# Kernel tuning notes

Hardware: AMD Instinct MI355X
Metric: run time of the kernel (lower is better)

The kernel has to match this reference:

```python
import jax, jax.numpy as jnp
import numpy as np
from jax import lax

B, C, H, W = 32, 3, 128, 128
HP, WP = 7, 7          # feature map after 4 stride-2 valid 3x3 convs on 128
GH, GW = 32, 32        # glimpse shape
BN_EPS = 1e-5


def _conv(x, w, b, stride):
    y = lax.conv_general_dilated(x, w, (stride, stride), 'VALID',
                                 dimension_numbers=('NCHW', 'OIHW', 'NCHW'))
    return y + b[None, :, None, None]


def _bn(x, g, be):
    # training-mode BatchNorm2d: biased batch stats over (N,H,W)
    m = x.mean(axis=(0, 2, 3), keepdims=True)
    v = ((x - m) ** 2).mean(axis=(0, 2, 3), keepdims=True)
    return g[None, :, None, None] * (x - m) * lax.rsqrt(v + BN_EPS) + be[None, :, None, None]


def setup_inputs() -> dict:
    key = jax.random.key(0)
    ks = jax.random.split(key, 16)
    def w_init(k, shape):
        fan_in = shape[1] * shape[2] * shape[3]
        return (jax.random.normal(k, shape, jnp.float32) / np.sqrt(fan_in)).astype(jnp.float32)
    chans = [3, 64, 64, 64, 64]
    inp = {}
    inp['img'] = jax.random.normal(ks[0], (B, C, H, W), jnp.float32)
    inp['eps_scale'] = jax.random.normal(ks[1], (B, HP, WP, 2), jnp.float32)
    inp['eps_shift'] = jax.random.normal(ks[2], (B, HP, WP, 2), jnp.float32)
    for i in range(4):
        inp[f'w{i+1}'] = w_init(ks[3 + i], (chans[i + 1], chans[i], 3, 3))
        inp[f'b{i+1}'] = jnp.zeros((chans[i + 1],), jnp.float32)
        inp[f'g{i+1}'] = jnp.ones((chans[i + 1],), jnp.float32)
        inp[f'be{i+1}'] = jnp.zeros((chans[i + 1],), jnp.float32)
    inp['wp'] = w_init(ks[10], (64, 64, 1, 1)); inp['bp'] = jnp.zeros((64,), jnp.float32)
    inp['wz'] = w_init(ks[11], (11, 64, 1, 1)); inp['bz'] = jnp.zeros((11,), jnp.float32)
    return inp


def reference(img, eps_scale, eps_shift,
              w1, b1, g1, be1, w2, b2, g2, be2,
              w3, b3, g3, be3, w4, b4, g4, be4,
              wp, bp, wz, bz):
    h = img
    for (w, b, g, be) in ((w1, b1, g1, be1), (w2, b2, g2, be2),
                          (w3, b3, g3, be3), (w4, b4, g4, be4)):
        h = jax.nn.elu(_bn(_conv(h, w, b, 2), g, be))
    feats = jax.nn.elu(_conv(h, wp, bp, 1))            # [B,64,HP,WP]

    # --- znet and latent splits (only scale/shift affect returned glimpses) ---
    Z = _conv(feats, wz, bz, 1).transpose(0, 2, 3, 1)  # [B,HP,WP,11]
    smean, slogstd = Z[..., 3:5], Z[..., 5:7]
    shmean, shlogstd = Z[..., 7:9], Z[..., 9:11]
    z_scale = smean + jax.nn.softplus(slogstd) * eps_scale
    z_shift = shmean + jax.nn.softplus(shlogstd) * eps_shift

    glimpse_hw = jnp.array([GH, GW], jnp.float32)
    image_hw = jnp.array([H, W], jnp.float32)
    fmap_hw = jnp.array([HP, WP], jnp.float32)
    scale_img = jax.nn.sigmoid(z_scale) * glimpse_hw / image_hw   # [B,HP,WP,2] (h,w)
    shift_img = jax.nn.sigmoid(z_shift) / fmap_hw                 # [B,HP,WP,2] (i,j)

    ii = jnp.arange(HP, dtype=jnp.float32) / HP
    jj = jnp.arange(WP, dtype=jnp.float32) / WP
    ij = jnp.stack(jnp.meshgrid(ii, jj, indexing='ij'), axis=-1)  # [HP,WP,2]
    center = (ij[None] + shift_img) * 2.0 - 1.0                   # [B,HP,WP,2] in [-1,1]

    K = HP * WP
    th = scale_img[..., 0].reshape(B, K)   # height scale
    tw = scale_img[..., 1].reshape(B, K)   # width scale
    tx = center[..., 0].reshape(B, K)      # row (y) center
    ty = center[..., 1].reshape(B, K)      # col (x) center

    # affine_grid (align_corners=False) base coords; theta = [[tw,0,ty],[0,th,tx]]
    xb = (2.0 * jnp.arange(GW, dtype=jnp.float32) + 1.0) / GW - 1.0
    yb = (2.0 * jnp.arange(GH, dtype=jnp.float32) + 1.0) / GH - 1.0
    ixn = tw[:, :, None, None] * xb[None, None, None, :] + ty[:, :, None, None]  # [B,K,1,GW]
    iyn = th[:, :, None, None] * yb[None, None, :, None] + tx[:, :, None, None]  # [B,K,GH,1]
    # normalized -> pixel coords (align_corners=False)
    px = jnp.broadcast_to(((ixn + 1.0) * W - 1.0) * 0.5, (B, K, GH, GW))
    py = jnp.broadcast_to(((iyn + 1.0) * H - 1.0) * 0.5, (B, K, GH, GW))

    def sample_one(im, pxb, pyb):
        # im [C,H,W]; pxb/pyb [K,GH,GW]; bilinear, zero padding
        x0 = jnp.floor(pxb); y0 = jnp.floor(pyb)
        wx1 = pxb - x0; wy1 = pyb - y0
        x0i = x0.astype(jnp.int32); y0i = y0.astype(jnp.int32)
        x1i = x0i + 1; y1i = y0i + 1
        def g(yi, xi):
            m = ((xi >= 0) & (xi < W) & (yi >= 0) & (yi < H)).astype(im.dtype)
            v = im[:, jnp.clip(yi, 0, H - 1), jnp.clip(xi, 0, W - 1)]  # [C,K,GH,GW]
            return v * m[None]
        return (g(y0i, x0i) * ((1 - wy1) * (1 - wx1))[None]
                + g(y0i, x1i) * ((1 - wy1) * wx1)[None]
                + g(y1i, x0i) * (wy1 * (1 - wx1))[None]
                + g(y1i, x1i) * (wy1 * wx1)[None])

    xs = jax.vmap(sample_one)(img, px, py)            # [B,C,K,GH,GW]
    return xs.transpose(0, 2, 1, 3, 4).reshape(B * K, C, GH, GW)
```

## Files before the change

kernel.cpp:

```cpp
#include <hip/hip_runtime.h>
#include <math.h>

#define BATCH 32

__device__ __forceinline__ float eluf(float v) { return v > 0.f ? v : expm1f(v); }
__device__ __forceinline__ float softplusf(float x) {
    return fmaxf(x, 0.f) + log1pf(expf(-fabsf(x)));
}
__device__ __forceinline__ float sigmoidf(float x) { return 1.f / (1.f + expf(-x)); }

__global__ __launch_bounds__(256) void wtrans_kernel(
    const float* __restrict__ w1, float* __restrict__ wt1,
    const float* __restrict__ w2, float* __restrict__ wt2,
    const float* __restrict__ w3, float* __restrict__ wt3,
    const float* __restrict__ w4, float* __restrict__ wt4)
{
    const int idx = blockIdx.x * 256 + threadIdx.x;
    const float* w; float* wt; int cin;
    switch (blockIdx.y) {
        case 0:  w = w1; wt = wt1; cin = 3;  break;
        case 1:  w = w2; wt = wt2; cin = 64; break;
        case 2:  w = w3; wt = wt3; cin = 64; break;
        default: w = w4; wt = wt4; cin = 64; break;
    }
    if (idx < cin * 576) {
        const int k = idx % 9, rest = idx / 9;
        const int co = rest & 63, ci = rest >> 6;
        wt[idx] = w[(co * cin + ci) * 9 + k];
    }
}

__global__ __launch_bounds__(256, 2) void conv1_kernel(
    const float* __restrict__ in, const float* __restrict__ wt,
    const float* __restrict__ bias, float* __restrict__ out)
{
    const int b  = blockIdx.x;
    const int t  = threadIdx.x;
    const int px = blockIdx.z * 256 + t;
    const bool active = px < 63 * 63;
    const int p = active ? px : 0;
    const int y = p / 63, x = p % 63;

    const float* ib = in + (size_t)b * 3 * 128 * 128 + (2 * y) * 128 + 2 * x;

    float pch[27];
#pragma unroll
    for (int ci = 0; ci < 3; ++ci) {
        const float* ip = ib + ci * 128 * 128;
        float2 a0 = *(const float2*)(ip);
        float2 a1 = *(const float2*)(ip + 128);
        float2 a2 = *(const float2*)(ip + 256);
        pch[ci * 9 + 0] = a0.x; pch[ci * 9 + 1] = a0.y; pch[ci * 9 + 2] = ip[2];
        pch[ci * 9 + 3] = a1.x; pch[ci * 9 + 4] = a1.y; pch[ci * 9 + 5] = ip[130];
        pch[ci * 9 + 6] = a2.x; pch[ci * 9 + 7] = a2.y; pch[ci * 9 + 8] = ip[258];
    }

    float acc[64];
#pragma unroll
    for (int u = 0; u < 64; ++u) acc[u] = bias[u];

#pragma unroll 1
    for (int ci = 0; ci < 3; ++ci) {
        const float* wc = wt + ci * 576;
#pragma unroll
        for (int u = 0; u < 64; ++u)
#pragma unroll
            for (int k = 0; k < 9; ++k)
                acc[u] = fmaf(pch[ci * 9 + k], wc[u * 9 + k], acc[u]);
    }

    if (active) {
#pragma unroll
        for (int u = 0; u < 64; ++u)
            out[((size_t)(b * 64 + u) * 63 + y) * 64 + x] = acc[u];
    }
}

template <int CIN, int HIN, int RSIN, int HOUT, int WOUT, int RSOUT, int G, int BLOCK, int WPE>
__global__ __launch_bounds__(BLOCK, WPE) void conv_kernel(
    const float* __restrict__ in, const float* __restrict__ wt,
    const float* __restrict__ bias, float* __restrict__ out)
{
    const int b   = blockIdx.x;
    const int co0 = blockIdx.y * G;
    const int t   = threadIdx.x;
    const int px  = blockIdx.z * BLOCK + t;
    const bool active = px < HOUT * WOUT;
    const int p = active ? px : 0;
    const int y = p / WOUT, x = p % WOUT;

    const float* ib = in + (size_t)b * CIN * HIN * RSIN + (2 * y) * RSIN + 2 * x;

    float acc[G];
#pragma unroll
    for (int u = 0; u < G; ++u) acc[u] = bias[co0 + u];

#pragma unroll 1
    for (int ci = 0; ci < CIN; ci += 2) {
        const float* ipA = ib + (size_t)ci * (HIN * RSIN);
        const float* ipB = ipA + (HIN * RSIN);
        float2 aA0 = *(const float2*)(ipA);
        float2 aA1 = *(const float2*)(ipA + RSIN);
        float2 aA2 = *(const float2*)(ipA + 2 * RSIN);
        float  cA0 = ipA[2], cA1 = ipA[RSIN + 2], cA2 = ipA[2 * RSIN + 2];
        float2 aB0 = *(const float2*)(ipB);
        float2 aB1 = *(const float2*)(ipB + RSIN);
        float2 aB2 = *(const float2*)(ipB + 2 * RSIN);
        float  cB0 = ipB[2], cB1 = ipB[RSIN + 2], cB2 = ipB[2 * RSIN + 2];

        const float pA[9] = {aA0.x, aA0.y, cA0, aA1.x, aA1.y, cA1, aA2.x, aA2.y, cA2};
        const float pB[9] = {aB0.x, aB0.y, cB0, aB1.x, aB1.y, cB1, aB2.x, aB2.y, cB2};

        const float* wcA = wt + (size_t)ci * 576 + co0 * 9;
        const float* wcB = wcA + 576;
#pragma unroll
        for (int u = 0; u < G; ++u)
#pragma unroll
            for (int j = 0; j < 9; ++j)
                acc[u] = fmaf(pA[j], wcA[u * 9 + j], acc[u]);
#pragma unroll
        for (int u = 0; u < G; ++u)
#pragma unroll
            for (int j = 0; j < 9; ++j)
                acc[u] = fmaf(pB[j], wcB[u * 9 + j], acc[u]);
    }

    if (active) {
#pragma unroll
        for (int u = 0; u < G; ++u)
            out[((size_t)(b * 64 + co0 + u) * HOUT + y) * RSOUT + x] = acc[u];
    }
}

template <int PLANE_PAD, int RSOUT, int BPS>
__global__ __launch_bounds__(256) void stats_kernel(
    const float* __restrict__ h, float* __restrict__ partial)
{
    const int c = blockIdx.x, sp = blockIdx.y, t = threadIdx.x;
    constexpr int N4 = PLANE_PAD / 4;
    constexpr int Q  = RSOUT / 4;
    float s = 0.f, q = 0.f;
    for (int bb = sp * BPS; bb < (sp + 1) * BPS; ++bb) {
        const float4* pp = (const float4*)(h + (size_t)(bb * 64 + c) * PLANE_PAD);
        for (int i = t; i < N4; i += 256) {
            float4 v = pp[i];
            float w_ = ((i & (Q - 1)) == (Q - 1)) ? 0.f : v.w;
            s += v.x + v.y + v.z + w_;
            q += v.x * v.x + v.y * v.y + v.z * v.z + w_ * w_;
        }
    }
    __shared__ float ls[4], lq[4];
    const int lane = t & 63, wv = t >> 6;
#pragma unroll
    for (int off = 32; off > 0; off >>= 1) {
        s += __shfl_down(s, off);
        q += __shfl_down(q, off);
    }
    if (lane == 0) { ls[wv] = s; lq[wv] = q; }
    __syncthreads();
    if (t == 0) {
        s = ls[0] + ls[1] + ls[2] + ls[3];
        q = lq[0] + lq[1] + lq[2] + lq[3];
        partial[(sp * 64 + c) * 2 + 0] = s;
        partial[(sp * 64 + c) * 2 + 1] = q;
    }
}

template <int PLANE_PAD, int NREAL>
__global__ __launch_bounds__(256) void bnelu_kernel(
    float* __restrict__ h, const float* __restrict__ partial,
    const float* __restrict__ g, const float* __restrict__ be)
{
    __shared__ float sa[64], sb[64];
    const int t = threadIdx.x;
    if (t < 64) {
        float s = 0.f, q = 0.f;
#pragma unroll
        for (int k = 0; k < 8; ++k) {
            s += partial[(k * 64 + t) * 2 + 0];
            q += partial[(k * 64 + t) * 2 + 1];
        }
        constexpr float invN = 1.f / (float)(BATCH * NREAL);
        float m = s * invN;
        float var = fmaf(q, invN, -m * m);
        float a = g[t] * rsqrtf(var + 1e-5f);
        sa[t] = a;
        sb[t] = fmaf(-a, m, be[t]);
    }
    __syncthreads();

    const long long total4 = (long long)BATCH * 64 * PLANE_PAD / 4;
    float4* h4 = (float4*)h;
    for (long long i4 = (long long)blockIdx.x * 256 + t; i4 < total4;
         i4 += (long long)gridDim.x * 256) {
        int c = (int)((i4 * 4 / PLANE_PAD) & 63);
        float a = sa[c], bb = sb[c];
        float4 v = h4[i4];
        v.x = eluf(fmaf(a, v.x, bb));
        v.y = eluf(fmaf(a, v.y, bb));
        v.z = eluf(fmaf(a, v.z, bb));
        v.w = eluf(fmaf(a, v.w, bb));
        h4[i4] = v;
    }
}

__global__ __launch_bounds__(256) void head_kernel(
    const float* __restrict__ x4, const float* __restrict__ partial4,
    const float* __restrict__ g4, const float* __restrict__ be4,
    const float* __restrict__ wp, const float* __restrict__ bp,
    const float* __restrict__ wz, const float* __restrict__ bz,
    const float* __restrict__ eps_scale, const float* __restrict__ eps_shift,
    float* __restrict__ params)
{
    __shared__ float xs[64 * 49];
    __shared__ float fe[64 * 49];
    __shared__ float zz[11 * 49];
    __shared__ float ha[64], hb[64];
    const int b = blockIdx.x, t = threadIdx.x;

    if (t < 64) {
        float s = 0.f, q = 0.f;
#pragma unroll
        for (int k = 0; k < 8; ++k) {
            s += partial4[(k * 64 + t) * 2 + 0];
            q += partial4[(k * 64 + t) * 2 + 1];
        }
        constexpr float invN = 1.f / (float)(BATCH * 49);
        float m = s * invN;
        float var = fmaf(q, invN, -m * m);
        float a = g4[t] * rsqrtf(var + 1e-5f);
        ha[t] = a;
        hb[t] = fmaf(-a, m, be4[t]);
    }
    __syncthreads();

    for (int i = t; i < 64 * 49; i += 256) {
        int c = i / 49, p = i % 49;
        float v = x4[(size_t)b * 64 * 56 + c * 56 + (p / 7) * 8 + (p % 7)];
        xs[i] = eluf(fmaf(ha[c], v, hb[c]));
    }
    __syncthreads();

    for (int i = t; i < 64 * 49; i += 256) {
        int co = i / 49, p = i % 49;
        float a = bp[co];
        for (int ci = 0; ci < 64; ++ci) a = fmaf(xs[ci * 49 + p], wp[co * 64 + ci], a);
        fe[i] = eluf(a);
    }
    __syncthreads();

    for (int i = t; i < 11 * 49; i += 256) {
        int co = i / 49, p = i % 49;
        float a = bz[co];
        for (int ci = 0; ci < 64; ++ci) a = fmaf(fe[ci * 49 + p], wz[co * 64 + ci], a);
        zz[i] = a;
    }
    __syncthreads();

    if (t < 49) {
        const int i = t / 7, j = t % 7;
        float es0 = eps_scale[((size_t)b * 49 + t) * 2 + 0];
        float es1 = eps_scale[((size_t)b * 49 + t) * 2 + 1];
        float eh0 = eps_shift[((size_t)b * 49 + t) * 2 + 0];
        float eh1 = eps_shift[((size_t)b * 49 + t) * 2 + 1];
        float zs0 = zz[3 * 49 + t] + softplusf(zz[5 * 49 + t]) * es0;
        float zs1 = zz[4 * 49 + t] + softplusf(zz[6 * 49 + t]) * es1;
        float zh0 = zz[7 * 49 + t] + softplusf(zz[9 * 49 + t]) * eh0;
        float zh1 = zz[8 * 49 + t] + softplusf(zz[10 * 49 + t]) * eh1;
        float th = sigmoidf(zs0) * 0.25f;
        float tw = sigmoidf(zs1) * 0.25f;
        float tx = ((float)i / 7.0f + sigmoidf(zh0) / 7.0f) * 2.f - 1.f;
        float ty = ((float)j / 7.0f + sigmoidf(zh1) / 7.0f) * 2.f - 1.f;
        float4* pp = (float4*)params;
        pp[b * 49 + t] = make_float4(th, tw, tx, ty);
    }
}

__device__ __forceinline__ float tap(const float* __restrict__ im, int yy, int xx) {
    bool ok = (xx >= 0) & (xx < 128) & (yy >= 0) & (yy < 128);
    int yc = min(max(yy, 0), 127);
    int xc = min(max(xx, 0), 127);
    return ok ? im[yc * 128 + xc] : 0.f;
}

__global__ __launch_bounds__(256) void sampler_kernel(
    const float* __restrict__ img, const float* __restrict__ params,
    float* __restrict__ out)
{
    const int bk = blockIdx.x;
    const int b  = bk / 49;
    const float4 pr = ((const float4*)params)[bk];
    const float th = pr.x, tw = pr.y, tx = pr.z, ty = pr.w;

    for (int idx = threadIdx.x; idx < 3072; idx += 256) {
        const int c  = idx >> 10;
        const int gy = (idx >> 5) & 31;
        const int gx = idx & 31;
        float xb = (2.f * gx + 1.f) / 32.f - 1.f;
        float yb = (2.f * gy + 1.f) / 32.f - 1.f;
        float ixn = fmaf(tw, xb, ty);
        float iyn = fmaf(th, yb, tx);
        float px = ((ixn + 1.f) * 128.f - 1.f) * 0.5f;
        float py = ((iyn + 1.f) * 128.f - 1.f) * 0.5f;
        float x0f = floorf(px), y0f = floorf(py);
        float wx = px - x0f, wy = py - y0f;
        int x0 = (int)x0f, y0 = (int)y0f;
        const float* im = img + ((size_t)b * 3 + c) * 16384;
        float v00 = tap(im, y0, x0);
        float v01 = tap(im, y0, x0 + 1);
        float v10 = tap(im, y0 + 1, x0);
        float v11 = tap(im, y0 + 1, x0 + 1);
        float r = v00 * (1.f - wy) * (1.f - wx) + v01 * (1.f - wy) * wx +
                  v10 * wy * (1.f - wx)        + v11 * wy * wx;
        out[(size_t)bk * 3072 + idx] = r;
    }
}

extern "C" void kernel_launch(void* const* d_in, const int* in_sizes, int n_in,
                              void* d_out, int out_size, void* d_ws, size_t ws_size,
                              hipStream_t stream)
{
    const float* img       = (const float*)d_in[0];
    const float* eps_scale = (const float*)d_in[1];
    const float* eps_shift = (const float*)d_in[2];
    const float* w1 = (const float*)d_in[3],  *b1 = (const float*)d_in[4];
    const float* g1 = (const float*)d_in[5],  *be1 = (const float*)d_in[6];
    const float* w2 = (const float*)d_in[7],  *b2 = (const float*)d_in[8];
    const float* g2 = (const float*)d_in[9],  *be2 = (const float*)d_in[10];
    const float* w3 = (const float*)d_in[11], *b3 = (const float*)d_in[12];
    const float* g3 = (const float*)d_in[13], *be3 = (const float*)d_in[14];
    const float* w4 = (const float*)d_in[15], *b4 = (const float*)d_in[16];
    const float* g4 = (const float*)d_in[17], *be4 = (const float*)d_in[18];
    const float* wp = (const float*)d_in[19], *bp = (const float*)d_in[20];
    const float* wz = (const float*)d_in[21], *bz = (const float*)d_in[22];

    float* ws     = (float*)d_ws;
    float* params = ws;
    float* part1  = ws + 8192;
    float* part2  = ws + 9216;
    float* part3  = ws + 10240;
    float* part4  = ws + 11264;
    float* wt1    = ws + 16384;
    float* wt2    = ws + 20480;
    float* wt3    = ws + 57344;
    float* wt4    = ws + 94208;
    float* h1     = ws + 131072;
    float* h2     = h1 + (size_t)32 * 64 * 63 * 64;
    float* h3     = h2 + (size_t)32 * 64 * 31 * 32;
    float* h4     = h3 + (size_t)32 * 64 * 15 * 16;

    float* outp = (float*)d_out;

    wtrans_kernel<<<dim3(144, 4), 256, 0, stream>>>(w1, wt1, w2, wt2, w3, wt3, w4, wt4);

    conv1_kernel<<<dim3(32, 1, 16), 256, 0, stream>>>(img, wt1, b1, h1);
    stats_kernel<63 * 64, 64, 4><<<dim3(64, 8), 256, 0, stream>>>(h1, part1);
    bnelu_kernel<63 * 64, 63 * 63><<<2048, 256, 0, stream>>>(h1, part1, g1, be1);

    conv_kernel<64, 63, 64, 31, 31, 32, 8, 256, 4>
        <<<dim3(32, 8, 4), 256, 0, stream>>>(h1, wt2, b2, h2);
    stats_kernel<31 * 32, 32, 4><<<dim3(64, 8), 256, 0, stream>>>(h2, part2);
    bnelu_kernel<31 * 32, 31 * 31><<<1984, 256, 0, stream>>>(h2, part2, g2, be2);

    conv_kernel<64, 31, 32, 15, 15, 16, 2, 256, 4>
        <<<dim3(32, 32, 1), 256, 0, stream>>>(h2, wt3, b3, h3);
    stats_kernel<15 * 16, 16, 4><<<dim3(64, 8), 256, 0, stream>>>(h3, part3);
    bnelu_kernel<15 * 16, 15 * 15><<<480, 256, 0, stream>>>(h3, part3, g3, be3);

    conv_kernel<64, 15, 16, 7, 7, 8, 1, 64, 8>
        <<<dim3(32, 64, 1), 64, 0, stream>>>(h3, wt4, b4, h4);
    stats_kernel<7 * 8, 8, 4><<<dim3(64, 8), 256, 0, stream>>>(h4, part4);

    head_kernel<<<32, 256, 0, stream>>>(h4, part4, g4, be4, wp, bp, wz, bz,
                                        eps_scale, eps_shift, params);

    sampler_kernel<<<1568, 256, 0, stream>>>(img, params, outp);
}
```

Measured before the change: 194.5 us.

## Stage conv2 input rows in LDS via async global_load_lds double buffering

Replaces the generic conv2 launch with a dedicated kernel that copies 17-row strips of four input channels at a time into shared memory using direct global-to-LDS loads, double-buffered so the next channel group loads while the current one is computed. Each block now covers 8 output rows and 16 output channels (previously 8 channels over a flat pixel range), so input is fetched once per block and patches are read from LDS instead of global memory. The cost is extra shared memory and barriers per iteration, one idle lane column per row, and reliance on the global_load_lds builtin with its alignment and ordering rules.

```diff
diff --git a/kernel.cpp b/kernel.cpp
--- a/kernel.cpp
+++ b/kernel.cpp
@@ -8,6 +8,12 @@
     return fmaxf(x, 0.f) + log1pf(expf(-fabsf(x)));
 }
 __device__ __forceinline__ float sigmoidf(float x) { return 1.f / (1.f + expf(-x)); }
+
+__device__ __forceinline__ void gload16(const float* g, float* l) {
+    __builtin_amdgcn_global_load_lds(
+        (const __attribute__((address_space(1))) void*)g,
+        (__attribute__((address_space(3))) void*)l, 16, 0, 0);
+}
 
 __global__ __launch_bounds__(256) void wtrans_kernel(
     const float* __restrict__ w1, float* __restrict__ wt1,
@@ -73,6 +79,72 @@
 #pragma unroll
         for (int u = 0; u < 64; ++u)
             out[((size_t)(b * 64 + u) * 63 + y) * 64 + x] = acc[u];
+    }
+}
+
+__global__ __launch_bounds__(256) void conv2_kernel(
+    const float* __restrict__ in, const float* __restrict__ wt,
+    const float* __restrict__ bias, float* __restrict__ out)
+{
+    __shared__ float tile[2][4][1088];
+    const int b   = blockIdx.x;
+    const int co0 = blockIdx.y * 16;
+    const int y0  = blockIdx.z * 8;
+    const int t   = threadIdx.x;
+    const int wv  = t >> 6, lane = t & 63;
+
+    const int ty_r = t >> 5, tx_r = t & 31;
+    const bool active = (tx_r < 31) && (y0 + ty_r < 31);
+    const int ty = active ? ty_r : 0;
+    const int tx = active ? tx_r : 0;
+
+    float acc[16];
+#pragma unroll
+    for (int u = 0; u < 16; ++u) acc[u] = bias[co0 + u];
+
+    const float* src_base = in + (size_t)(b * 64 + wv) * 4032 + 2 * y0 * 64;
+
+#define STAGE(buf, k)                                                        \
+    {                                                                        \
+        const float* s_ = src_base + (size_t)(k) * 4 * 4032;                 \
+        float* d_ = &tile[buf][wv][0];                                       \
+        _Pragma("unroll")                                                    \
+        for (int i_ = 0; i_ < 4; ++i_)                                       \
+            gload16(s_ + i_ * 256 + lane * 4, d_ + i_ * 256);                \
+        if (lane < 16) gload16(s_ + 1024 + lane * 4, d_ + 1024);             \
+    }
+
+    STAGE(0, 0)
+    __syncthreads();
+
+#pragma unroll 1
+    for (int k = 0; k < 16; ++k) {
+        const int cur = k & 1;
+        if (k < 15) STAGE(cur ^ 1, k + 1)
+
+#pragma unroll
+        for (int ch = 0; ch < 4; ++ch) {
+            const float* tp = &tile[cur][ch][2 * ty * 64 + 2 * tx];
+            float2 a0 = *(const float2*)(tp);
+            float2 a1 = *(const float2*)(tp + 64);
+            float2 a2 = *(const float2*)(tp + 128);
+            const float pch[9] = {a0.x, a0.y, tp[2], a1.x, a1.y, tp[66],
+                                  a2.x, a2.y, tp[130]};
+            const float* wc = wt + (size_t)(k * 4 + ch) * 576 + co0 * 9;
+#pragma unroll
+            for (int u = 0; u < 16; ++u)
+#pragma unroll
+                for (int j = 0; j < 9; ++j)
+                    acc[u] = fmaf(pch[j], wc[u * 9 + j], acc[u]);
+        }
+        __syncthreads();
+    }
+#undef STAGE
+
+    if (active) {
+#pragma unroll
+        for (int u = 0; u < 16; ++u)
+            out[((size_t)(b * 64 + co0 + u) * 31 + (y0 + ty)) * 32 + tx] = acc[u];
     }
 }
 
@@ -357,8 +429,7 @@
     stats_kernel<63 * 64, 64, 4><<<dim3(64, 8), 256, 0, stream>>>(h1, part1);
     bnelu_kernel<63 * 64, 63 * 63><<<2048, 256, 0, stream>>>(h1, part1, g1, be1);
 
-    conv_kernel<64, 63, 64, 31, 31, 32, 8, 256, 4>
-        <<<dim3(32, 8, 4), 256, 0, stream>>>(h1, wt2, b2, h2);
+    conv2_kernel<<<dim3(32, 4, 4), 256, 0, stream>>>(h1, wt2, b2, h2);
     stats_kernel<31 * 32, 32, 4><<<dim3(64, 8), 256, 0, stream>>>(h2, part2);
     bnelu_kernel<31 * 32, 31 * 31><<<1984, 256, 0, stream>>>(h2, part2, g2, be2);
 
```

Result: slower. 277.1 us (+42.5%).

## Fuse BN+ELU into next conv input and BN stats into conv epilogue

Applied to the files above, without the earlier changes.

Removes the separate bnelu and most stats kernels. Each conv now rebuilds the previous layer's BN scale and shift from partial sums, applies BN+ELU to its input patches as it loads them, and writes per-block channel sum and sum-of-squares partials in its epilogue. This drops several full read/write passes over the activations and several kernel launches. In exchange, ELU is recomputed for every overlapping patch load (about 2.25x for 3x3 stride 2), and layer 2 must reduce 128 partials per channel on entry.

```diff
diff --git a/kernel.cpp b/kernel.cpp
--- a/kernel.cpp
+++ b/kernel.cpp
@@ -76,14 +76,72 @@
     }
 }
 
-template <int CIN, int HIN, int RSIN, int HOUT, int WOUT, int RSOUT, int G, int BLOCK, int WPE>
-__global__ __launch_bounds__(BLOCK, WPE) void conv_kernel(
+template <int PLANE_PAD, int RSOUT, int BPS>
+__global__ __launch_bounds__(256) void stats_kernel(
+    const float* __restrict__ h, float* __restrict__ partial)
+{
+    const int c = blockIdx.x, sp = blockIdx.y, t = threadIdx.x;
+    constexpr int N4 = PLANE_PAD / 4;
+    constexpr int Q  = RSOUT / 4;
+    float s = 0.f, q = 0.f;
+    for (int bb = sp * BPS; bb < (sp + 1) * BPS; ++bb) {
+        const float4* pp = (const float4*)(h + (size_t)(bb * 64 + c) * PLANE_PAD);
+        for (int i = t; i < N4; i += 256) {
+            float4 v = pp[i];
+            float w_ = ((i & (Q - 1)) == (Q - 1)) ? 0.f : v.w;
+            s += v.x + v.y + v.z + w_;
+            q += v.x * v.x + v.y * v.y + v.z * v.z + w_ * w_;
+        }
+    }
+    __shared__ float ls[4], lq[4];
+    const int lane = t & 63, wv = t >> 6;
+#pragma unroll
+    for (int off = 32; off > 0; off >>= 1) {
+        s += __shfl_down(s, off);
+        q += __shfl_down(q, off);
+    }
+    if (lane == 0) { ls[wv] = s; lq[wv] = q; }
+    __syncthreads();
+    if (t == 0) {
+        s = ls[0] + ls[1] + ls[2] + ls[3];
+        q = lq[0] + lq[1] + lq[2] + lq[3];
+        partial[(sp * 64 + c) * 2 + 0] = s;
+        partial[(sp * 64 + c) * 2 + 1] = q;
+    }
+}
+
+template <int CIN, int HIN, int RSIN, int HOUT, int WOUT, int RSOUT, int G, int BLOCK,
+          int WPE, int PIN, int NREAL_IN, int NZ>
+__global__ __launch_bounds__(BLOCK, WPE) void convf_kernel(
     const float* __restrict__ in, const float* __restrict__ wt,
-    const float* __restrict__ bias, float* __restrict__ out)
-{
+    const float* __restrict__ bias,
+    const float* __restrict__ pin, const float* __restrict__ g,
+    const float* __restrict__ be,
+    float* __restrict__ out, float* __restrict__ pout)
+{
+    constexpr int NW = BLOCK / 64;
+    __shared__ float bna[64], bnb[64];
+    __shared__ float red_s[NW][G], red_q[NW][G];
+
     const int b   = blockIdx.x;
     const int co0 = blockIdx.y * G;
     const int t   = threadIdx.x;
+
+    if (t < 64) {
+        float s = 0.f, q = 0.f;
+        for (int k = 0; k < PIN; ++k) {
+            s += pin[(k * 64 + t) * 2 + 0];
+            q += pin[(k * 64 + t) * 2 + 1];
+        }
+        constexpr float invN = 1.f / (float)(BATCH * NREAL_IN);
+        float m = s * invN;
+        float var = fmaf(q, invN, -m * m);
+        float a = g[t] * rsqrtf(var + 1e-5f);
+        bna[t] = a;
+        bnb[t] = fmaf(-a, m, be[t]);
+    }
+    __syncthreads();
+
     const int px  = blockIdx.z * BLOCK + t;
     const bool active = px < HOUT * WOUT;
     const int p = active ? px : 0;
@@ -108,8 +166,16 @@
         float2 aB2 = *(const float2*)(ipB + 2 * RSIN);
         float  cB0 = ipB[2], cB1 = ipB[RSIN + 2], cB2 = ipB[2 * RSIN + 2];
 
-        const float pA[9] = {aA0.x, aA0.y, cA0, aA1.x, aA1.y, cA1, aA2.x, aA2.y, cA2};
-        const float pB[9] = {aB0.x, aB0.y, cB0, aB1.x, aB1.y, cB1, aB2.x, aB2.y, cB2};
+        const float aA = bna[ci], bA = bnb[ci];
+        const float aB = bna[ci + 1], bB = bnb[ci + 1];
+
+        float pA[9] = {aA0.x, aA0.y, cA0, aA1.x, aA1.y, cA1, aA2.x, aA2.y, cA2};
+        float pB[9] = {aB0.x, aB0.y, cB0, aB1.x, aB1.y, cB1, aB2.x, aB2.y, cB2};
+#pragma unroll
+        for (int j = 0; j < 9; ++j) {
+            pA[j] = eluf(fmaf(aA, pA[j], bA));
+            pB[j] = eluf(fmaf(aB, pB[j], bB));
+        }
 
         const float* wcA = wt + (size_t)ci * 576 + co0 * 9;
         const float* wcB = wcA + 576;
@@ -125,82 +191,28 @@
                 acc[u] = fmaf(pB[j], wcB[u * 9 + j], acc[u]);
     }
 
-    if (active) {
-#pragma unroll
-        for (int u = 0; u < G; ++u)
-            out[((size_t)(b * 64 + co0 + u) * HOUT + y) * RSOUT + x] = acc[u];
-    }
-}
-
-template <int PLANE_PAD, int RSOUT, int BPS>
-__global__ __launch_bounds__(256) void stats_kernel(
-    const float* __restrict__ h, float* __restrict__ partial)
-{
-    const int c = blockIdx.x, sp = blockIdx.y, t = threadIdx.x;
-    constexpr int N4 = PLANE_PAD / 4;
-    constexpr int Q  = RSOUT / 4;
-    float s = 0.f, q = 0.f;
-    for (int bb = sp * BPS; bb < (sp + 1) * BPS; ++bb) {
-        const float4* pp = (const float4*)(h + (size_t)(bb * 64 + c) * PLANE_PAD);
-        for (int i = t; i < N4; i += 256) {
-            float4 v = pp[i];
-            float w_ = ((i & (Q - 1)) == (Q - 1)) ? 0.f : v.w;
-            s += v.x + v.y + v.z + w_;
-            q += v.x * v.x + v.y * v.y + v.z * v.z + w_ * w_;
-        }
-    }
-    __shared__ float ls[4], lq[4];
     const int lane = t & 63, wv = t >> 6;
 #pragma unroll
-    for (int off = 32; off > 0; off >>= 1) {
-        s += __shfl_down(s, off);
-        q += __shfl_down(q, off);
-    }
-    if (lane == 0) { ls[wv] = s; lq[wv] = q; }
-    __syncthreads();
-    if (t == 0) {
-        s = ls[0] + ls[1] + ls[2] + ls[3];
-        q = lq[0] + lq[1] + lq[2] + lq[3];
-        partial[(sp * 64 + c) * 2 + 0] = s;
-        partial[(sp * 64 + c) * 2 + 1] = q;
-    }
-}
-
-template <int PLANE_PAD, int NREAL>
-__global__ __launch_bounds__(256) void bnelu_kernel(
-    float* __restrict__ h, const float* __restrict__ partial,
-    const float* __restrict__ g, const float* __restrict__ be)
-{
-    __shared__ float sa[64], sb[64];
-    const int t = threadIdx.x;
-    if (t < 64) {
-        float s = 0.f, q = 0.f;
-#pragma unroll
-        for (int k = 0; k < 8; ++k) {
-            s += partial[(k * 64 + t) * 2 + 0];
-            q += partial[(k * 64 + t) * 2 + 1];
-        }
-        constexpr float invN = 1.f / (float)(BATCH * NREAL);
-        float m = s * invN;
-        float var = fmaf(q, invN, -m * m);
-        float a = g[t] * rsqrtf(var + 1e-5f);
-        sa[t] = a;
-        sb[t] = fmaf(-a, m, be[t]);
-    }
-    __syncthreads();
-
-    const long long total4 = (long long)BATCH * 64 * PLANE_PAD / 4;
-    float4* h4 = (float4*)h;
-    for (long long i4 = (long long)blockIdx.x * 256 + t; i4 < total4;
-         i4 += (long long)gridDim.x * 256) {
-        int c = (int)((i4 * 4 / PLANE_PAD) & 63);
-        float a = sa[c], bb = sb[c];
-        float4 v = h4[i4];
-        v.x = eluf(fmaf(a, v.x, bb));
-        v.y = eluf(fmaf(a, v.y, bb));
-        v.z = eluf(fmaf(a, v.z, bb));
-        v.w = eluf(fmaf(a, v.w, bb));
-        h4[i4] = v;
+    for (int u = 0; u < G; ++u) {
+        float v = active ? acc[u] : 0.f;
+        if (active)
+            out[((size_t)(b * 64 + co0 + u) * HOUT + y) * RSOUT + x] = v;
+        float s = v, q = v * v;
+#pragma unroll
+        for (int off = 32; off > 0; off >>= 1) {
+            s += __shfl_down(s, off);
+            q += __shfl_down(q, off);
+        }
+        if (lane == 0) { red_s[wv][u] = s; red_q[wv][u] = q; }
+    }
+    __syncthreads();
+    if (t < 2 * G) {
+        const int u = t % G;
+        const bool wantq = t >= G;
+        float tt = 0.f;
+#pragma unroll
+        for (int k = 0; k < NW; ++k) tt += wantq ? red_q[k][u] : red_s[k][u];
+        pout[((b * NZ + blockIdx.z) * 64 + co0 + u) * 2 + (wantq ? 1 : 0)] = tt;
     }
 }
 
@@ -221,7 +233,7 @@
     if (t < 64) {
         float s = 0.f, q = 0.f;
 #pragma unroll
-        for (int k = 0; k < 8; ++k) {
+        for (int k = 0; k < 32; ++k) {
             s += partial4[(k * 64 + t) * 2 + 0];
             q += partial4[(k * 64 + t) * 2 + 1];
         }
@@ -337,14 +349,14 @@
     float* ws     = (float*)d_ws;
     float* params = ws;
     float* part1  = ws + 8192;
-    float* part2  = ws + 9216;
-    float* part3  = ws + 10240;
-    float* part4  = ws + 11264;
-    float* wt1    = ws + 16384;
-    float* wt2    = ws + 20480;
-    float* wt3    = ws + 57344;
-    float* wt4    = ws + 94208;
-    float* h1     = ws + 131072;
+    float* part2  = ws + 16384;
+    float* part3  = ws + 32768;
+    float* part4  = ws + 40960;
+    float* wt1    = ws + 49152;
+    float* wt2    = ws + 53248;
+    float* wt3    = ws + 90112;
+    float* wt4    = ws + 126976;
+    float* h1     = ws + 163840;
     float* h2     = h1 + (size_t)32 * 64 * 63 * 64;
     float* h3     = h2 + (size_t)32 * 64 * 31 * 32;
     float* h4     = h3 + (size_t)32 * 64 * 15 * 16;
@@ -355,21 +367,15 @@
 
     conv1_kernel<<<dim3(32, 1, 16), 256, 0, stream>>>(img, wt1, b1, h1);
     stats_kernel<63 * 64, 64, 4><<<dim3(64, 8), 256, 0, stream>>>(h1, part1);
-    bnelu_kernel<63 * 64, 63 * 63><<<2048, 256, 0, stream>>>(h1, part1, g1, be1);
-
-    conv_kernel<64, 63, 64, 31, 31, 32, 8, 256, 4>
-        <<<dim3(32, 8, 4), 256, 0, stream>>>(h1, wt2, b2, h2);
-    stats_kernel<31 * 32, 32, 4><<<dim3(64, 8), 256, 0, stream>>>(h2, part2);
-    bnelu_kernel<31 * 32, 31 * 31><<<1984, 256, 0, stream>>>(h2, part2, g2, be2);
-
-    conv_kernel<64, 31, 32, 15, 15, 16, 2, 256, 4>
-        <<<dim3(32, 32, 1), 256, 0, stream>>>(h2, wt3, b3, h3);
-    stats_kernel<15 * 16, 16, 4><<<dim3(64, 8), 256, 0, stream>>>(h3, part3);
-    bnelu_kernel<15 * 16, 15 * 15><<<480, 256, 0, stream>>>(h3, part3, g3, be3);
-
-    conv_kernel<64, 15, 16, 7, 7, 8, 1, 64, 8>
-        <<<dim3(32, 64, 1), 64, 0, stream>>>(h3, wt4, b4, h4);
-    stats_kernel<7 * 8, 8, 4><<<dim3(64, 8), 256, 0, stream>>>(h4, part4);
+
+    convf_kernel<64, 63, 64, 31, 31, 32, 8, 256, 4, 8, 63 * 63, 4>
+        <<<dim3(32, 8, 4), 256, 0, stream>>>(h1, wt2, b2, part1, g1, be1, h2, part2);
+
+    convf_kernel<64, 31, 32, 15, 15, 16, 2, 256, 4, 128, 31 * 31, 1>
+        <<<dim3(32, 32, 1), 256, 0, stream>>>(h2, wt3, b3, part2, g2, be2, h3, part3);
+
+    convf_kernel<64, 15, 16, 7, 7, 8, 1, 64, 8, 32, 15 * 15, 1>
+        <<<dim3(32, 64, 1), 64, 0, stream>>>(h3, wt4, b4, part3, g3, be3, h4, part4);
 
     head_kernel<<<32, 256, 0, stream>>>(h4, part4, g4, be4, wp, bp, wz, bz,
                                         eps_scale, eps_shift, params);
```

After: 338.1 us. 1.74x slower.

## Split conv2 input-channel reduction across two launches and sum partials downstream

Applied to the files above, without the earlier changes.

Conv2 is split into two kernel launches, each reducing over half of the input channels and writing to its own buffer (h2a, h2b). The stats and BN+ELU kernels gain a DUAL mode that adds the two partial buffers before computing statistics and applying the activation. The intent is to shorten each conv's serial reduction loop. Because the launches sit on the same stream they run one after the other, so the change mainly adds an extra partial-output write and an extra read in the stats and bnelu passes.

```diff
diff --git a/kernel.cpp b/kernel.cpp
--- a/kernel.cpp
+++ b/kernel.cpp
@@ -76,7 +76,8 @@
     }
 }
 
-template <int CIN, int HIN, int RSIN, int HOUT, int WOUT, int RSOUT, int G, int BLOCK, int WPE>
+template <int CIN, int HIN, int RSIN, int HOUT, int WOUT, int RSOUT, int G, int BLOCK,
+          int WPE, int CI_B, int CI_E, bool FIRST>
 __global__ __launch_bounds__(BLOCK, WPE) void conv_kernel(
     const float* __restrict__ in, const float* __restrict__ wt,
     const float* __restrict__ bias, float* __restrict__ out)
@@ -93,10 +94,10 @@
 
     float acc[G];
 #pragma unroll
-    for (int u = 0; u < G; ++u) acc[u] = bias[co0 + u];
+    for (int u = 0; u < G; ++u) acc[u] = FIRST ? bias[co0 + u] : 0.f;
 
 #pragma unroll 1
-    for (int ci = 0; ci < CIN; ci += 2) {
+    for (int ci = CI_B; ci < CI_E; ci += 2) {
         const float* ipA = ib + (size_t)ci * (HIN * RSIN);
         const float* ipB = ipA + (HIN * RSIN);
         float2 aA0 = *(const float2*)(ipA);
@@ -132,9 +133,10 @@
     }
 }
 
-template <int PLANE_PAD, int RSOUT, int BPS>
+template <int PLANE_PAD, int RSOUT, int BPS, bool DUAL>
 __global__ __launch_bounds__(256) void stats_kernel(
-    const float* __restrict__ h, float* __restrict__ partial)
+    const float* __restrict__ h, const float* __restrict__ h2,
+    float* __restrict__ partial)
 {
     const int c = blockIdx.x, sp = blockIdx.y, t = threadIdx.x;
     constexpr int N4 = PLANE_PAD / 4;
@@ -142,8 +144,13 @@
     float s = 0.f, q = 0.f;
     for (int bb = sp * BPS; bb < (sp + 1) * BPS; ++bb) {
         const float4* pp = (const float4*)(h + (size_t)(bb * 64 + c) * PLANE_PAD);
+        const float4* p2 = (const float4*)(h2 + (size_t)(bb * 64 + c) * PLANE_PAD);
         for (int i = t; i < N4; i += 256) {
             float4 v = pp[i];
+            if (DUAL) {
+                float4 w2 = p2[i];
+                v.x += w2.x; v.y += w2.y; v.z += w2.z; v.w += w2.w;
+            }
             float w_ = ((i & (Q - 1)) == (Q - 1)) ? 0.f : v.w;
             s += v.x + v.y + v.z + w_;
             q += v.x * v.x + v.y * v.y + v.z * v.z + w_ * w_;
@@ -166,9 +173,10 @@
     }
 }
 
-template <int PLANE_PAD, int NREAL>
+template <int PLANE_PAD, int NREAL, bool DUAL>
 __global__ __launch_bounds__(256) void bnelu_kernel(
-    float* __restrict__ h, const float* __restrict__ partial,
+    float* __restrict__ h, const float* __restrict__ h2,
+    const float* __restrict__ partial,
     const float* __restrict__ g, const float* __restrict__ be)
 {
     __shared__ float sa[64], sb[64];
@@ -191,11 +199,16 @@
 
     const long long total4 = (long long)BATCH * 64 * PLANE_PAD / 4;
     float4* h4 = (float4*)h;
+    const float4* hb4 = (const float4*)h2;
     for (long long i4 = (long long)blockIdx.x * 256 + t; i4 < total4;
          i4 += (long long)gridDim.x * 256) {
         int c = (int)((i4 * 4 / PLANE_PAD) & 63);
         float a = sa[c], bb = sb[c];
         float4 v = h4[i4];
+        if (DUAL) {
+            float4 w2 = hb4[i4];
+            v.x += w2.x; v.y += w2.y; v.z += w2.z; v.w += w2.w;
+        }
         v.x = eluf(fmaf(a, v.x, bb));
         v.y = eluf(fmaf(a, v.y, bb));
         v.z = eluf(fmaf(a, v.z, bb));
@@ -345,8 +358,9 @@
     float* wt3    = ws + 57344;
     float* wt4    = ws + 94208;
     float* h1     = ws + 131072;
-    float* h2     = h1 + (size_t)32 * 64 * 63 * 64;
-    float* h3     = h2 + (size_t)32 * 64 * 31 * 32;
+    float* h2a    = h1 + (size_t)32 * 64 * 63 * 64;
+    float* h2b    = h2a + (size_t)32 * 64 * 31 * 32;
+    float* h3     = h2b + (size_t)32 * 64 * 31 * 32;
     float* h4     = h3 + (size_t)32 * 64 * 15 * 16;
 
     float* outp = (float*)d_out;
@@ -354,22 +368,24 @@
     wtrans_kernel<<<dim3(144, 4), 256, 0, stream>>>(w1, wt1, w2, wt2, w3, wt3, w4, wt4);
 
     conv1_kernel<<<dim3(32, 1, 16), 256, 0, stream>>>(img, wt1, b1, h1);
-    stats_kernel<63 * 64, 64, 4><<<dim3(64, 8), 256, 0, stream>>>(h1, part1);
-    bnelu_kernel<63 * 64, 63 * 63><<<2048, 256, 0, stream>>>(h1, part1, g1, be1);
-
-    conv_kernel<64, 63, 64, 31, 31, 32, 8, 256, 4>
-        <<<dim3(32, 8, 4), 256, 0, stream>>>(h1, wt2, b2, h2);
-    stats_kernel<31 * 32, 32, 4><<<dim3(64, 8), 256, 0, stream>>>(h2, part2);
-    bnelu_kernel<31 * 32, 31 * 31><<<1984, 256, 0, stream>>>(h2, part2, g2, be2);
-
-    conv_kernel<64, 31, 32, 15, 15, 16, 2, 256, 4>
-        <<<dim3(32, 32, 1), 256, 0, stream>>>(h2, wt3, b3, h3);
-    stats_kernel<15 * 16, 16, 4><<<dim3(64, 8), 256, 0, stream>>>(h3, part3);
-    bnelu_kernel<15 * 16, 15 * 15><<<480, 256, 0, stream>>>(h3, part3, g3, be3);
-
-    conv_kernel<64, 15, 16, 7, 7, 8, 1, 64, 8>
+    stats_kernel<63 * 64, 64, 4, false><<<dim3(64, 8), 256, 0, stream>>>(h1, h1, part1);
+    bnelu_kernel<63 * 64, 63 * 63, false><<<2048, 256, 0, stream>>>(h1, h1, part1, g1, be1);
+
+    conv_kernel<64, 63, 64, 31, 31, 32, 8, 256, 4, 0, 32, true>
+        <<<dim3(32, 8, 4), 256, 0, stream>>>(h1, wt2, b2, h2a);
+    conv_kernel<64, 63, 64, 31, 31, 32, 8, 256, 4, 32, 64, false>
+        <<<dim3(32, 8, 4), 256, 0, stream>>>(h1, wt2, b2, h2b);
+    stats_kernel<31 * 32, 32, 4, true><<<dim3(64, 8), 256, 0, stream>>>(h2a, h2b, part2);
+    bnelu_kernel<31 * 32, 31 * 31, true><<<1984, 256, 0, stream>>>(h2a, h2b, part2, g2, be2);
+
+    conv_kernel<64, 31, 32, 15, 15, 16, 2, 256, 4, 0, 64, true>
+        <<<dim3(32, 32, 1), 256, 0, stream>>>(h2a, wt3, b3, h3);
+    stats_kernel<15 * 16, 16, 4, false><<<dim3(64, 8), 256, 0, stream>>>(h3, h3, part3);
+    bnelu_kernel<15 * 16, 15 * 15, false><<<480, 256, 0, stream>>>(h3, h3, part3, g3, be3);
+
+    conv_kernel<64, 15, 16, 7, 7, 8, 1, 64, 8, 0, 64, true>
         <<<dim3(32, 64, 1), 64, 0, stream>>>(h3, wt4, b4, h4);
-    stats_kernel<7 * 8, 8, 4><<<dim3(64, 8), 256, 0, stream>>>(h4, part4);
+    stats_kernel<7 * 8, 8, 4, false><<<dim3(64, 8), 256, 0, stream>>>(h4, h4, part4);
 
     head_kernel<<<32, 256, 0, stream>>>(h4, part4, g4, be4, wp, bp, wz, bz,
                                         eps_scale, eps_shift, params);
```

Result: slower. 199.4 us (+2.5%).
